# Kernel optimization log

Hardware: AMD Instinct MI355X
Metric: run time of the kernel (lower is better)

The kernel has to match this reference:

```python
import jax, jax.numpy as jnp
import numpy as np

N = 32768        # nodes (512 boards x 64 squares)
E_PER = 16384    # edges per edge type
T = 8            # edge types
IN = 16          # in_channels
H = 4            # attention heads
DIMS = (32, 128, 512)  # hidden_dim1, hidden_dim2, out_dim
NEG = 0.2        # LeakyReLU slope (PyG GATConv default)


def _glorot(key, shape):
    fan = shape[0] + shape[-1]
    return jax.random.uniform(key, shape, jnp.float32, -1.0, 1.0) * np.sqrt(6.0 / fan)


def setup_inputs() -> dict:
    key = jax.random.key(0)
    ki = iter(jax.random.split(key, 40))
    inp = {}
    inp["x"] = jax.random.normal(next(ki), (N, IN), jnp.float32)
    inp["edge_index_types"] = jax.random.randint(next(ki), (T, 2, E_PER), 0, N)
    in_dims = (IN,) + DIMS[:2]
    for l, (din, dout) in enumerate(zip(in_dims, DIMS), start=1):
        inp[f"W{l}"] = _glorot(next(ki), (din, H * dout))
        inp[f"We{l}"] = _glorot(next(ki), (T, H * dout))
        inp[f"asrc{l}"] = _glorot(next(ki), (H, dout))
        inp[f"adst{l}"] = _glorot(next(ki), (H, dout))
        inp[f"aedge{l}"] = _glorot(next(ki), (H, dout))
        inp[f"b{l}"] = jnp.zeros((dout,), jnp.float32)
    return inp


def _gat(h, src, dst, ea, W, We, a_src, a_dst, a_edge, b, dout):
    """One GATConv(heads=H, concat=False, edge_dim=T), inference (no dropout)."""
    hp = (h @ W).reshape(-1, H, dout)                 # [N,H,C]
    ep = (ea @ We).reshape(-1, H, dout)               # [E,H,C]
    alpha = ((hp * a_src).sum(-1)[src]
             + (hp * a_dst).sum(-1)[dst]
             + (ep * a_edge).sum(-1))                 # [E,H]
    alpha = jax.nn.leaky_relu(alpha, NEG)
    # scatter-softmax over incoming edges of each dst node
    m = jax.ops.segment_max(alpha, dst, num_segments=N)
    ex = jnp.exp(alpha - m[dst])
    denom = jax.ops.segment_sum(ex, dst, num_segments=N)
    w = ex / denom[dst]                               # [E,H]
    msg = hp[src] * w[:, :, None]                     # [E,H,C]
    out = jax.ops.segment_sum(msg, dst, num_segments=N)  # [N,H,C]
    return out.mean(axis=1) + b                       # concat=False -> head mean


def reference(x, edge_index_types, W1, We1, asrc1, adst1, aedge1, b1,
              W2, We2, asrc2, adst2, aedge2, b2,
              W3, We3, asrc3, adst3, aedge3, b3):
    # chess_graph_to_single: merge 8 edge lists, one-hot edge type attr
    ei = jnp.transpose(edge_index_types, (1, 0, 2)).reshape(2, T * E_PER)
    ea = jnp.repeat(jnp.eye(T, dtype=x.dtype), E_PER, axis=0)  # [T*E_PER, T]
    # PyG GATConv add_self_loops=True, fill_value='mean' for edge_attr
    loops = jnp.arange(N)
    src = jnp.concatenate([ei[0], loops])
    dst = jnp.concatenate([ei[1], loops])
    ea = jnp.concatenate([ea, jnp.broadcast_to(ea.mean(0), (N, T))], axis=0)

    h = jax.nn.relu(_gat(x, src, dst, ea, W1, We1, asrc1, adst1, aedge1, b1, DIMS[0]))
    h = jax.nn.relu(_gat(h, src, dst, ea, W2, We2, asrc2, adst2, aedge2, b2, DIMS[1]))
    return _gat(h, src, dst, ea, W3, We3, asrc3, adst3, aedge3, b3, DIMS[2])
```

## Files before the change

kernel.cpp:

```cpp
#include <hip/hip_runtime.h>
#include <hip/hip_bf16.h>
#include <math.h>

#define N_NODES 32768
#define E_PER   16384
#define T_TYPES 8
#define E_TYPED (T_TYPES * E_PER)
#define E_TOT   (E_TYPED + N_NODES)
#define NEG_SLOPE 0.2f
#define CSR_CAP 64

typedef _Float16 f16x8 __attribute__((ext_vector_type(8)));
typedef float f32x4 __attribute__((ext_vector_type(4)));

__device__ __forceinline__ float tof(float v) { return v; }
__device__ __forceinline__ float tof(_Float16 v) { return (float)v; }
__device__ __forceinline__ float lrelu(float a) { return a > 0.0f ? a : NEG_SLOPE * a; }

__device__ __forceinline__ void osm_upd(float& m, float& z, float a) {
  if (a > m) { z = z * __expf(m - a) + 1.0f; m = a; }
  else       { z += __expf(a - m); }
}
__device__ __forceinline__ void osm_comb(float& m, float& z, int off) {
  float om = __shfl_xor(m, off, 64);
  float oz = __shfl_xor(z, off, 64);
  float nm = fmaxf(m, om);
  z = z * __expf(m - nm) + oz * __expf(om - nm);
  m = nm;
}

__device__ __forceinline__ void gload16(const void* g, void* l) {
  __builtin_amdgcn_global_load_lds(
      (const __attribute__((address_space(1))) void*)g,
      (__attribute__((address_space(3))) void*)l,
      16, 0, 0);
}

__device__ void prep_blk(int b, const float* __restrict__ W, const float* __restrict__ We,
                         const float* __restrict__ asrc, const float* __restrict__ adst,
                         const float* __restrict__ aedge, float* __restrict__ prep,
                         int din, int dout) {
  int task = b * 4 + (threadIdx.x >> 6);
  int lane = threadIdx.x & 63;
  int hd = 4 * din;
  float s = 0.0f;
  if (task < 2 * hd) {
    int k = (task < hd) ? task : task - hd;
    int h = k / din, i = k % din;
    const float* a = (task < hd) ? asrc : adst;
    for (int c = lane; c < dout; c += 64)
      s += W[(size_t)i * 4 * dout + h * dout + c] * a[h * dout + c];
#pragma unroll
    for (int off = 32; off >= 1; off >>= 1) s += __shfl_xor(s, off, 64);
    if (lane == 0) prep[((task < hd) ? 0 : 512) + h * 128 + i] = s;
  } else if (task < 2 * hd + 32) {
    int k = task - 2 * hd; int t = k >> 2, h = k & 3;
    for (int c = lane; c < dout; c += 64)
      s += We[(size_t)t * 4 * dout + h * dout + c] * aedge[h * dout + c];
#pragma unroll
    for (int off = 32; off >= 1; off >>= 1) s += __shfl_xor(s, off, 64);
    if (lane == 0) prep[1024 + t * 4 + h] = s;
  } else if (task < 2 * hd + 36) {
    int h = task - 2 * hd - 32;
    for (int t = 0; t < 8; ++t)
      for (int c = lane; c < dout; c += 64)
        s += We[(size_t)t * 4 * dout + h * dout + c] * aedge[h * dout + c];
#pragma unroll
    for (int off = 32; off >= 1; off >>= 1) s += __shfl_xor(s, off, 64);
    if (lane == 0) prep[1024 + 32 + h] = s * 0.125f;
  }
}

__device__ void wt_blk(int jt, int kt, const float* __restrict__ W,
                       _Float16* __restrict__ Bt, int din, int dout) {
  __shared__ float Tt[64][65];
  int jb = jt * 64, kb = kt * 64;
  int KK = 4 * din;
  int tx = threadIdx.x & 63, ty4 = threadIdx.x >> 6;
  for (int r0 = 0; r0 < 64; r0 += 4) {
    int r = r0 + ty4;
    int k = kb + r, h = k / din, i = k % din;
    Tt[r][tx] = W[(size_t)i * 4 * dout + h * dout + jb + tx];
  }
  __syncthreads();
  for (int r0 = 0; r0 < 64; r0 += 4) {
    int r = r0 + ty4;
    Bt[(size_t)(jb + r) * KK + kb + tx] = (_Float16)Tt[tx][r];
  }
}

#define NB_P1 41
#define NB_P2 73
#define NB_P3 265
#define NB_W2 4
#define NB_W3 64
#define NB_Z  32
#define NB_WEIGHTS (NB_P1 + NB_P2 + NB_P3 + NB_W2 + NB_W3 + NB_Z)

__global__ __launch_bounds__(256) void k_weights(
    const float* __restrict__ W1, const float* __restrict__ We1,
    const float* __restrict__ as1, const float* __restrict__ ad1, const float* __restrict__ ae1,
    const float* __restrict__ W2, const float* __restrict__ We2,
    const float* __restrict__ as2, const float* __restrict__ ad2, const float* __restrict__ ae2,
    const float* __restrict__ W3, const float* __restrict__ We3,
    const float* __restrict__ as3, const float* __restrict__ ad3, const float* __restrict__ ae3,
    float* __restrict__ prep1, float* __restrict__ prep2, float* __restrict__ prep3,
    _Float16* __restrict__ w2t, _Float16* __restrict__ w3t, int* __restrict__ cnt) {
  int b = blockIdx.x;
  if (b < NB_P1) { prep_blk(b, W1, We1, as1, ad1, ae1, prep1, 16, 32); return; }
  b -= NB_P1;
  if (b < NB_P2) { prep_blk(b, W2, We2, as2, ad2, ae2, prep2, 32, 128); return; }
  b -= NB_P2;
  if (b < NB_P3) { prep_blk(b, W3, We3, as3, ad3, ae3, prep3, 128, 512); return; }
  b -= NB_P3;
  if (b < NB_W2) { wt_blk(b & 1, b >> 1, W2, w2t, 32, 128); return; }
  b -= NB_W2;
  if (b < NB_W3) { wt_blk(b & 7, b >> 3, W3, w3t, 128, 512); return; }
  b -= NB_W3;
  int4 z; z.x = z.y = z.z = z.w = 0;
  reinterpret_cast<int4*>(cnt)[b * 256 + threadIdx.x] = z;
}

__global__ __launch_bounds__(256) void k_fill_s1(const int* __restrict__ ei, int* __restrict__ cnt,
                                                 int* __restrict__ csr,
                                                 const float* __restrict__ x,
                                                 const float* __restrict__ prep1,
                                                 float* __restrict__ s_src,
                                                 float* __restrict__ s_dst) {
  int b = blockIdx.x;
  if (b < E_TOT / 256) {
    int e = b * 256 + threadIdx.x;
    int src, dst, t;
    if (e < E_TYPED) { t = e >> 14; int j = e & (E_PER - 1); src = ei[2 * t * E_PER + j]; dst = ei[(2 * t + 1) * E_PER + j]; }
    else { src = dst = e - E_TYPED; t = 8; }
    dst &= (N_NODES - 1);
    int pos = atomicAdd(cnt + dst, 1);
    if (pos < CSR_CAP)
      csr[dst * CSR_CAP + pos] = (src & (N_NODES - 1)) | (t << 16);
    return;
  }
  __shared__ float vv[128];
  int tid = threadIdx.x;
  for (int j = tid; j < 128; j += 256) {
    int s = j / 16, i = j % 16;
    vv[j] = prep1[(s & 3) * 128 + i + ((s >= 4) ? 512 : 0)];
  }
  __syncthreads();
  int lane = tid & 63, wv = tid >> 6;
  int n = (b - E_TOT / 256) * 4 + wv;
  const float* row = x + (size_t)n * 16;
  float p0 = 0, p1 = 0, p2 = 0, p3 = 0, p4 = 0, p5 = 0, p6 = 0, p7 = 0;
  for (int c = lane; c < 16; c += 64) {
    float v = row[c];
    p0 += v * vv[0 * 16 + c]; p1 += v * vv[1 * 16 + c];
    p2 += v * vv[2 * 16 + c]; p3 += v * vv[3 * 16 + c];
    p4 += v * vv[4 * 16 + c]; p5 += v * vv[5 * 16 + c];
    p6 += v * vv[6 * 16 + c]; p7 += v * vv[7 * 16 + c];
  }
#pragma unroll
  for (int off = 32; off >= 1; off >>= 1) {
    p0 += __shfl_xor(p0, off, 64); p1 += __shfl_xor(p1, off, 64);
    p2 += __shfl_xor(p2, off, 64); p3 += __shfl_xor(p3, off, 64);
    p4 += __shfl_xor(p4, off, 64); p5 += __shfl_xor(p5, off, 64);
    p6 += __shfl_xor(p6, off, 64); p7 += __shfl_xor(p7, off, 64);
  }
  if (lane == 0) {
    float* a = s_src + (size_t)n * 4; a[0] = p0; a[1] = p1; a[2] = p2; a[3] = p3;
    float* bq = s_dst + (size_t)n * 4; bq[0] = p4; bq[1] = p5; bq[2] = p6; bq[3] = p7;
  }
}

template <typename TI, int DIN, typename TO>
__global__ __launch_bounds__(256) void k_attn_agg(const TI* __restrict__ hin,
                                                  const int* __restrict__ csr,
                                                  const int* __restrict__ cnt,
                                                  const float* __restrict__ prep,
                                                  const float* __restrict__ s_src,
                                                  const float* __restrict__ s_dst,
                                                  TO* __restrict__ agg) {
  constexpr int ACC = (4 * DIN) / 64;
  __shared__ float se[68];
  int tid = threadIdx.x, lane = tid & 63, wv = tid >> 6;
  for (int j = tid; j < 68; j += 256) se[j] = (j < 36) ? prep[1024 + j] : 0.0f;
  __syncthreads();
  int n = blockIdx.x * 4 + wv;
  int o0 = n * CSR_CAP;
  int kd = cnt[n];
  kd = max(0, min(kd, CSR_CAP));
  const float* sdp = s_dst + (size_t)n * 4;
  float sd0 = sdp[0], sd1 = sdp[1], sd2 = sdp[2], sd3 = sdp[3];

  float m0 = -1e30f, m1 = -1e30f, m2 = -1e30f, m3 = -1e30f;
  float z0 = 0, z1 = 0, z2 = 0, z3 = 0;
  for (int i = lane; i < kd; i += 64) {
    int ent = csr[o0 + i];
    int sx = ent & (N_NODES - 1);
    int tt = (ent >> 16) & 15;
    const float4 sv = *reinterpret_cast<const float4*>(s_src + (size_t)sx * 4);
    float a0 = lrelu(sv.x + sd0 + se[tt * 4 + 0]);
    float a1 = lrelu(sv.y + sd1 + se[tt * 4 + 1]);
    float a2 = lrelu(sv.z + sd2 + se[tt * 4 + 2]);
    float a3 = lrelu(sv.w + sd3 + se[tt * 4 + 3]);
    osm_upd(m0, z0, a0); osm_upd(m1, z1, a1); osm_upd(m2, z2, a2); osm_upd(m3, z3, a3);
  }
#pragma unroll
  for (int off = 32; off >= 1; off >>= 1) {
    osm_comb(m0, z0, off); osm_comb(m1, z1, off);
    osm_comb(m2, z2, off); osm_comb(m3, z3, off);
  }
  float r0 = (z0 > 0.0f) ? 1.0f / z0 : 0.0f;
  float r1 = (z1 > 0.0f) ? 1.0f / z1 : 0.0f;
  float r2 = (z2 > 0.0f) ? 1.0f / z2 : 0.0f;
  float r3 = (z3 > 0.0f) ? 1.0f / z3 : 0.0f;

  float acc[ACC];
#pragma unroll
  for (int q = 0; q < ACC; ++q) acc[q] = 0.0f;

  for (int b0 = 0; b0 < kd; b0 += 64) {
    int i = b0 + lane;
    int sx = 0; float w0 = 0, w1 = 0, w2 = 0, w3 = 0;
    if (i < kd) {
      int ent = csr[o0 + i];
      sx = ent & (N_NODES - 1);
      int tt = (ent >> 16) & 15;
      const float4 sv = *reinterpret_cast<const float4*>(s_src + (size_t)sx * 4);
      w0 = __expf(lrelu(sv.x + sd0 + se[tt * 4 + 0]) - m0) * r0;
      w1 = __expf(lrelu(sv.y + sd1 + se[tt * 4 + 1]) - m1) * r1;
      w2 = __expf(lrelu(sv.z + sd2 + se[tt * 4 + 2]) - m2) * r2;
      w3 = __expf(lrelu(sv.w + sd3 + se[tt * 4 + 3]) - m3) * r3;
    }
    int cnt_ = min(64, kd - b0);
    for (int e = 0; e < cnt_; ++e) {
      int se_ = __shfl(sx, e, 64);
      float u0 = __shfl(w0, e, 64), u1 = __shfl(w1, e, 64);
      float u2 = __shfl(w2, e, 64), u3 = __shfl(w3, e, 64);
      if constexpr (DIN == 128) {
        unsigned int ru = *reinterpret_cast<const unsigned int*>(
            reinterpret_cast<const char*>(hin) + (size_t)se_ * 256 + 4 * lane);
        union { unsigned int u; _Float16 h[2]; } cv; cv.u = ru;
        float v0 = (float)cv.h[0], v1 = (float)cv.h[1];
        acc[0] += u0 * v0; acc[1] += u0 * v1;
        acc[2] += u1 * v0; acc[3] += u1 * v1;
        acc[4] += u2 * v0; acc[5] += u2 * v1;
        acc[6] += u3 * v0; acc[7] += u3 * v1;
      } else if constexpr (DIN == 32) {
        const TI* row = hin + (size_t)se_ * DIN;
        float v = tof(row[lane & 31]);
        bool hi = lane >= 32;
        float wa = hi ? u1 : u0;
        float wb = hi ? u3 : u2;
        acc[0] += wa * v; acc[1] += wb * v;
      } else {
        const TI* row = hin + (size_t)se_ * DIN;
        float v = tof(row[lane & 15]);
        int hh = lane >> 4;
        float wa = (hh == 0) ? u0 : (hh == 1) ? u1 : (hh == 2) ? u2 : u3;
        acc[0] += wa * v;
      }
    }
  }

  TO* ar = agg + (size_t)n * (4 * DIN);
  if constexpr (DIN == 128) {
#pragma unroll
    for (int h = 0; h < 4; ++h) {
      ar[h * 128 + 2 * lane]     = (TO)acc[2 * h];
      ar[h * 128 + 2 * lane + 1] = (TO)acc[2 * h + 1];
    }
  } else if constexpr (DIN == 32) {
    ar[lane]      = (TO)acc[0];
    ar[64 + lane] = (TO)acc[1];
  } else {
    ar[lane] = (TO)acc[0];
  }
}

__global__ __launch_bounds__(128) void k_gemm1_s2(const float* __restrict__ A,
                                                  const float* __restrict__ W,
                                                  const float* __restrict__ bias,
                                                  const float* __restrict__ prep2,
                                                  float* __restrict__ out,
                                                  float* __restrict__ s_src,
                                                  float* __restrict__ s_dst) {
  constexpr int BM = 64, BN = 32, BK = 16, TM = 4, TN = 4, NT = 128;
  constexpr int K = 64, DIN = 16, DOUT = 32;
  constexpr int LDA = BM + 4;
  constexpr int LDB = BN + 4;
  __shared__ __align__(16) float As[BK * LDA];
  __shared__ __align__(16) float Bs[BK * LDB];
  __shared__ float ot[64][33];
  const int tid = threadIdx.x;
  const int tx = tid % (BN / TN);
  const int ty = tid / (BN / TN);
  const int mb = blockIdx.y * BM;
  float acc[TM][TN] = {};
  constexpr int ITA = (BM * BK) / (NT * 4);
  constexpr int ITB = (BK * BN) / (NT * 4);
  for (int kb = 0; kb < K; kb += BK) {
#pragma unroll
    for (int it = 0; it < ITA; ++it) {
      int f = it * NT * 4 + tid * 4;
      int r = f / BK, c = f % BK;
      float4 u = *reinterpret_cast<const float4*>(A + (size_t)(mb + r) * K + kb + c);
      As[(c + 0) * LDA + r] = u.x;
      As[(c + 1) * LDA + r] = u.y;
      As[(c + 2) * LDA + r] = u.z;
      As[(c + 3) * LDA + r] = u.w;
    }
#pragma unroll
    for (int it = 0; it < ITB; ++it) {
      int f = it * NT * 4 + tid * 4;
      int kk = f / BN, jj = f % BN;
      int k = kb + kk; int h = k / DIN; int i = k % DIN;
      float4 u = *reinterpret_cast<const float4*>(W + (size_t)i * 4 * DOUT + h * DOUT + jj);
      Bs[kk * LDB + jj + 0] = u.x;
      Bs[kk * LDB + jj + 1] = u.y;
      Bs[kk * LDB + jj + 2] = u.z;
      Bs[kk * LDB + jj + 3] = u.w;
    }
    __syncthreads();
#pragma unroll
    for (int kk = 0; kk < BK; ++kk) {
      float a_[TM], b_[TN];
      float4 va = *reinterpret_cast<const float4*>(&As[kk * LDA + ty * TM]);
      a_[0] = va.x; a_[1] = va.y; a_[2] = va.z; a_[3] = va.w;
      float4 vb = *reinterpret_cast<const float4*>(&Bs[kk * LDB + tx * TN]);
      b_[0] = vb.x; b_[1] = vb.y; b_[2] = vb.z; b_[3] = vb.w;
#pragma unroll
      for (int ii = 0; ii < TM; ++ii)
#pragma unroll
        for (int jj = 0; jj < TN; ++jj)
          acc[ii][jj] = fmaf(a_[ii], b_[jj], acc[ii][jj]);
    }
    __syncthreads();
  }
#pragma unroll
  for (int ii = 0; ii < TM; ++ii) {
    int ml = ty * TM + ii;
#pragma unroll
    for (int jj = 0; jj < TN; ++jj) {
      int j = tx * TN + jj;
      float v = acc[ii][jj] * 0.25f + bias[j];
      v = fmaxf(v, 0.0f);
      if (!isfinite(v)) v = 0.0f;
      out[(size_t)(mb + ml) * DOUT + j] = v;
      ot[ml][j] = v;
    }
  }
  __syncthreads();
#pragma unroll
  for (int q = 0; q < 4; ++q) {
    int t = q * 128 + tid;
    int s = t & 7, row = t >> 3;
    const float* vp = prep2 + (s & 3) * 128 + ((s >= 4) ? 512 : 0);
    float p = 0.0f;
#pragma unroll
    for (int c = 0; c < 32; ++c) p += ot[row][c] * vp[c];
    int n = mb + row;
    if (s < 4) s_src[(size_t)n * 4 + s] = p;
    else       s_dst[(size_t)n * 4 + (s - 4)] = p;
  }
}

__global__ __launch_bounds__(256) void k_gemm2_s3(const _Float16* __restrict__ A,
                                                  const _Float16* __restrict__ Bt,
                                                  const float* __restrict__ bias,
                                                  const float* __restrict__ prep3,
                                                  _Float16* __restrict__ out,
                                                  float* __restrict__ s_src,
                                                  float* __restrict__ s_dst) {
  constexpr int K = 128, DOUT = 128, BM = 128, BK = 64;
  __shared__ _Float16 smem[128 * 136];
  _Float16* As = smem;
  _Float16* Bs = smem + 8192;
  const int tid = threadIdx.x;
  const int lane = tid & 63, wv = tid >> 6;
  const int quad = lane >> 4, l16 = lane & 15;
  const int wm = (wv >> 1) * 64, wn = (wv & 1) * 64;
  const int mb = blockIdx.y * BM;
  const int srow = lane >> 3;
  const int scolB = (lane & 7) * 16;

  f32x4 acc[4][4] = {};
  float bv[4];
#pragma unroll
  for (int fj = 0; fj < 4; ++fj) bv[fj] = bias[wn + fj * 16 + l16];

  for (int kb = 0; kb < K; kb += BK) {
    __syncthreads();
#pragma unroll
    for (int i = 0; i < 4; ++i) {
      int q = wv * 4 + i;
      int r = q * 8 + srow;
      gload16(reinterpret_cast<const char*>(A) + (size_t)(mb + r) * 256 + kb * 2 + scolB,
              &As[q * 512]);
      gload16(reinterpret_cast<const char*>(Bt) + (size_t)r * 256 + kb * 2 + scolB,
              &Bs[q * 512]);
    }
    __syncthreads();
#pragma unroll
    for (int h = 0; h < 2; ++h) {
      f16x8 af[4], bf[4];
#pragma unroll
      for (int f = 0; f < 4; ++f) {
        af[f] = *reinterpret_cast<const f16x8*>(&As[(wm + f * 16 + l16) * 64 + h * 32 + quad * 8]);
        bf[f] = *reinterpret_cast<const f16x8*>(&Bs[(wn + f * 16 + l16) * 64 + h * 32 + quad * 8]);
      }
#pragma unroll
      for (int fi = 0; fi < 4; ++fi)
#pragma unroll
        for (int fj = 0; fj < 4; ++fj)
          acc[fi][fj] = __builtin_amdgcn_mfma_f32_16x16x32_f16(af[fi], bf[fj], acc[fi][fj], 0, 0, 0);
    }
  }
  __syncthreads();
  _Float16* ot = smem;
#pragma unroll
  for (int fi = 0; fi < 4; ++fi)
#pragma unroll
    for (int reg = 0; reg < 4; ++reg) {
      int ml = wm + fi * 16 + quad * 4 + reg;
#pragma unroll
      for (int fj = 0; fj < 4; ++fj) {
        int j = wn + fj * 16 + l16;
        float v = acc[fi][fj][reg] * 0.25f + bv[fj];
        v = fmaxf(v, 0.0f);
        if (!isfinite(v)) v = 0.0f;
        _Float16 hv = (_Float16)v;
        out[(size_t)(mb + ml) * DOUT + j] = hv;
        ot[ml * 136 + j] = hv;
      }
    }
  __syncthreads();
#pragma unroll
  for (int q = 0; q < 4; ++q) {
    int t = q * 256 + tid;
    int s = t & 7, row = t >> 3;
    const float* vp = prep3 + (s & 3) * 128 + ((s >= 4) ? 512 : 0);
    float p = 0.0f;
#pragma unroll
    for (int c0 = 0; c0 < 128; c0 += 8) {
      f16x8 hv = *reinterpret_cast<const f16x8*>(&ot[row * 136 + c0]);
      float4 a0 = *reinterpret_cast<const float4*>(vp + c0);
      float4 a1 = *reinterpret_cast<const float4*>(vp + c0 + 4);
      p += (float)hv[0] * a0.x + (float)hv[1] * a0.y + (float)hv[2] * a0.z + (float)hv[3] * a0.w
         + (float)hv[4] * a1.x + (float)hv[5] * a1.y + (float)hv[6] * a1.z + (float)hv[7] * a1.w;
    }
    int n = mb + row;
    if (s < 4) s_src[(size_t)n * 4 + s] = p;
    else       s_dst[(size_t)n * 4 + (s - 4)] = p;
  }
}

template <int K, int DOUT, bool RELU, typename TO>
__global__ __launch_bounds__(256) void k_gemm_mfma64(const _Float16* __restrict__ A,
                                                     const _Float16* __restrict__ Bt,
                                                     const float* __restrict__ bias,
                                                     TO* __restrict__ out) {
  constexpr int BM = 128, BK = 64;
  __shared__ _Float16 As[128 * 64];
  __shared__ _Float16 Bs[128 * 64];
  const int tid = threadIdx.x;
  const int lane = tid & 63, wv = tid >> 6;
  const int quad = lane >> 4, l16 = lane & 15;
  const int wm = (wv >> 1) * 64, wn = (wv & 1) * 64;
  const int mb = blockIdx.y * BM, jb = blockIdx.x * BM;
  const int srow = lane >> 3;
  const int scolB = (lane & 7) * 16;
  constexpr int ROWB = K * 2;

  f32x4 acc[4][4] = {};
  float bv[4];
#pragma unroll
  for (int fj = 0; fj < 4; ++fj) bv[fj] = bias[jb + wn + fj * 16 + l16];

  for (int kb = 0; kb < K; kb += BK) {
    __syncthreads();
#pragma unroll
    for (int i = 0; i < 4; ++i) {
      int q = wv * 4 + i;
      int r = q * 8 + srow;
      gload16(reinterpret_cast<const char*>(A) + (size_t)(mb + r) * ROWB + kb * 2 + scolB,
              &As[q * 512]);
      gload16(reinterpret_cast<const char*>(Bt) + (size_t)(jb + r) * ROWB + kb * 2 + scolB,
              &Bs[q * 512]);
    }
    __syncthreads();
#pragma unroll
    for (int h = 0; h < 2; ++h) {
      f16x8 af[4], bf[4];
#pragma unroll
      for (int f = 0; f < 4; ++f) {
        af[f] = *reinterpret_cast<const f16x8*>(&As[(wm + f * 16 + l16) * 64 + h * 32 + quad * 8]);
        bf[f] = *reinterpret_cast<const f16x8*>(&Bs[(wn + f * 16 + l16) * 64 + h * 32 + quad * 8]);
      }
#pragma unroll
      for (int fi = 0; fi < 4; ++fi)
#pragma unroll
        for (int fj = 0; fj < 4; ++fj)
          acc[fi][fj] = __builtin_amdgcn_mfma_f32_16x16x32_f16(af[fi], bf[fj], acc[fi][fj], 0, 0, 0);
    }
  }
#pragma unroll
  for (int fi = 0; fi < 4; ++fi)
#pragma unroll
    for (int reg = 0; reg < 4; ++reg) {
      int m = mb + wm + fi * 16 + quad * 4 + reg;
#pragma unroll
      for (int fj = 0; fj < 4; ++fj) {
        int j = jb + wn + fj * 16 + l16;
        float v = acc[fi][fj][reg] * 0.25f + bv[fj];
        if (RELU) v = fmaxf(v, 0.0f);
        if (!isfinite(v)) v = 0.0f;
        out[(size_t)m * DOUT + j] = (TO)v;
      }
    }
}

extern "C" void kernel_launch(void* const* d_in, const int* in_sizes, int n_in,
                              void* d_out, int out_size, void* d_ws, size_t ws_size,
                              hipStream_t stream) {
  (void)in_sizes; (void)n_in; (void)out_size; (void)ws_size;
  const float* x   = (const float*)d_in[0];
  const int*   ei  = (const int*)d_in[1];
  const float* W1  = (const float*)d_in[2];
  const float* We1 = (const float*)d_in[3];
  const float* as1 = (const float*)d_in[4];
  const float* ad1 = (const float*)d_in[5];
  const float* ae1 = (const float*)d_in[6];
  const float* b1  = (const float*)d_in[7];
  const float* W2  = (const float*)d_in[8];
  const float* We2 = (const float*)d_in[9];
  const float* as2 = (const float*)d_in[10];
  const float* ad2 = (const float*)d_in[11];
  const float* ae2 = (const float*)d_in[12];
  const float* b2  = (const float*)d_in[13];
  const float* W3  = (const float*)d_in[14];
  const float* We3 = (const float*)d_in[15];
  const float* as3 = (const float*)d_in[16];
  const float* ad3 = (const float*)d_in[17];
  const float* ae3 = (const float*)d_in[18];
  const float* b3  = (const float*)d_in[19];

  char* p = (char*)d_ws;
  int* cnt       = (int*)(p + 0);
  int* csr       = (int*)(p + 131072);
  float* ssrc    = (float*)(p + 8519680);
  float* sdst    = (float*)(p + 9043968);
  float* prep1   = (float*)(p + 9568256);
  float* prep2   = (float*)(p + 9572864);
  float* prep3   = (float*)(p + 9577472);
  float* h1      = (float*)(p + 9582080);
  _Float16* h2   = (_Float16*)(p + 13776384);
  float* agg1    = (float*)(p + 22164992);
  _Float16* agg2 = (_Float16*)(p + 30553600);
  _Float16* agg3 = (_Float16*)(p + 38942208);
  _Float16* w2t  = (_Float16*)(p + 72496640);
  _Float16* w3t  = (_Float16*)(p + 72529408);

  k_weights<<<NB_WEIGHTS, 256, 0, stream>>>(W1, We1, as1, ad1, ae1,
                                            W2, We2, as2, ad2, ae2,
                                            W3, We3, as3, ad3, ae3,
                                            prep1, prep2, prep3, w2t, w3t, cnt);
  k_fill_s1<<<E_TOT / 256 + N_NODES / 4, 256, 0, stream>>>(ei, cnt, csr, x, prep1, ssrc, sdst);

  k_attn_agg<float, 16, float><<<N_NODES / 4, 256, 0, stream>>>(x, csr, cnt, prep1, ssrc, sdst, agg1);
  k_gemm1_s2<<<dim3(1, N_NODES / 64), 128, 0, stream>>>(agg1, W1, b1, prep2, h1, ssrc, sdst);

  k_attn_agg<float, 32, _Float16><<<N_NODES / 4, 256, 0, stream>>>(h1, csr, cnt, prep2, ssrc, sdst, agg2);
  k_gemm2_s3<<<dim3(1, N_NODES / 128), 256, 0, stream>>>(agg2, w2t, b2, prep3, h2, ssrc, sdst);

  k_attn_agg<_Float16, 128, _Float16><<<N_NODES / 4, 256, 0, stream>>>(h2, csr, cnt, prep3, ssrc, sdst, agg3);
  k_gemm_mfma64<512, 512, false, float>
      <<<dim3(4, N_NODES / 128), 256, 0, stream>>>(agg3, w3t, b3, (float*)d_out);
}
```

Measured before the change: 319.0 us.

## Fuse all GAT stages into one persistent kernel with grid barriers

Replaces the eight separate launches with one persistent kernel of 512 blocks that steps through weight prep, CSR build, and the three attention-aggregate plus GEMM layers, separated by software grid barriers. Layers 1 and 2 now run aggregation and the dense transform in the same block, so the agg1/agg2 intermediates never go to global memory. The attention scores are double-buffered so one layer's scores can be written while the previous layer's are still being read. This removes per-launch overhead and some global round trips, but it relies on all 512 blocks being resident at once and on spin-wait barriers, and the final GEMM switches to smaller 64-row tiles.

```diff
diff --git a/kernel.cpp b/kernel.cpp
--- a/kernel.cpp
+++ b/kernel.cpp
@@ -9,18 +9,13 @@
 #define E_TOT   (E_TYPED + N_NODES)
 #define NEG_SLOPE 0.2f
 #define CSR_CAP 64
+#define GRID 512
 
 typedef _Float16 f16x8 __attribute__((ext_vector_type(8)));
 typedef float f32x4 __attribute__((ext_vector_type(4)));
 
-__device__ __forceinline__ float tof(float v) { return v; }
-__device__ __forceinline__ float tof(_Float16 v) { return (float)v; }
 __device__ __forceinline__ float lrelu(float a) { return a > 0.0f ? a : NEG_SLOPE * a; }
 
-__device__ __forceinline__ void osm_upd(float& m, float& z, float a) {
-  if (a > m) { z = z * __expf(m - a) + 1.0f; m = a; }
-  else       { z += __expf(a - m); }
-}
 __device__ __forceinline__ void osm_comb(float& m, float& z, int off) {
   float om = __shfl_xor(m, off, 64);
   float oz = __shfl_xor(z, off, 64);
@@ -34,6 +29,21 @@
       (const __attribute__((address_space(1))) void*)g,
       (__attribute__((address_space(3))) void*)l,
       16, 0, 0);
+}
+
+__device__ __forceinline__ void gridbar(int* bar, int target) {
+  __threadfence();
+  __syncthreads();
+  if (threadIdx.x == 0) {
+    atomicAdd(bar, 1);
+    int it = 0;
+    while (__hip_atomic_load(bar, __ATOMIC_RELAXED, __HIP_MEMORY_SCOPE_AGENT) < target) {
+      __builtin_amdgcn_s_sleep(2);
+      if (++it > (1 << 24)) break;
+    }
+  }
+  __syncthreads();
+  __threadfence();
 }
 
 __device__ void prep_blk(int b, const float* __restrict__ W, const float* __restrict__ We,
@@ -72,21 +82,21 @@
 }
 
 __device__ void wt_blk(int jt, int kt, const float* __restrict__ W,
-                       _Float16* __restrict__ Bt, int din, int dout) {
-  __shared__ float Tt[64][65];
+                       _Float16* __restrict__ Bt, int din, int dout, float* T) {
   int jb = jt * 64, kb = kt * 64;
   int KK = 4 * din;
   int tx = threadIdx.x & 63, ty4 = threadIdx.x >> 6;
   for (int r0 = 0; r0 < 64; r0 += 4) {
     int r = r0 + ty4;
     int k = kb + r, h = k / din, i = k % din;
-    Tt[r][tx] = W[(size_t)i * 4 * dout + h * dout + jb + tx];
+    T[r * 65 + tx] = W[(size_t)i * 4 * dout + h * dout + jb + tx];
   }
   __syncthreads();
   for (int r0 = 0; r0 < 64; r0 += 4) {
     int r = r0 + ty4;
-    Bt[(size_t)(jb + r) * KK + kb + tx] = (_Float16)Tt[tx][r];
-  }
+    Bt[(size_t)(jb + r) * KK + kb + tx] = (_Float16)T[tx * 65 + r];
+  }
+  __syncthreads();
 }
 
 #define NB_P1 41
@@ -96,426 +106,436 @@
 #define NB_W3 64
 #define NB_Z  32
 #define NB_WEIGHTS (NB_P1 + NB_P2 + NB_P3 + NB_W2 + NB_W3 + NB_Z)
-
-__global__ __launch_bounds__(256) void k_weights(
+#define NB_FILL 640
+#define NB_S1 8192
+
+__global__ __launch_bounds__(256, 2) void k_mega(
+    const float* __restrict__ x, const int* __restrict__ ei,
     const float* __restrict__ W1, const float* __restrict__ We1,
     const float* __restrict__ as1, const float* __restrict__ ad1, const float* __restrict__ ae1,
+    const float* __restrict__ b1,
     const float* __restrict__ W2, const float* __restrict__ We2,
     const float* __restrict__ as2, const float* __restrict__ ad2, const float* __restrict__ ae2,
+    const float* __restrict__ b2,
     const float* __restrict__ W3, const float* __restrict__ We3,
     const float* __restrict__ as3, const float* __restrict__ ad3, const float* __restrict__ ae3,
+    const float* __restrict__ b3,
+    int* __restrict__ cnt, int* __restrict__ csr,
+    float* __restrict__ ssrcA, float* __restrict__ sdstA,
+    float* __restrict__ ssrcB, float* __restrict__ sdstB,
     float* __restrict__ prep1, float* __restrict__ prep2, float* __restrict__ prep3,
-    _Float16* __restrict__ w2t, _Float16* __restrict__ w3t, int* __restrict__ cnt) {
-  int b = blockIdx.x;
-  if (b < NB_P1) { prep_blk(b, W1, We1, as1, ad1, ae1, prep1, 16, 32); return; }
-  b -= NB_P1;
-  if (b < NB_P2) { prep_blk(b, W2, We2, as2, ad2, ae2, prep2, 32, 128); return; }
-  b -= NB_P2;
-  if (b < NB_P3) { prep_blk(b, W3, We3, as3, ad3, ae3, prep3, 128, 512); return; }
-  b -= NB_P3;
-  if (b < NB_W2) { wt_blk(b & 1, b >> 1, W2, w2t, 32, 128); return; }
-  b -= NB_W2;
-  if (b < NB_W3) { wt_blk(b & 7, b >> 3, W3, w3t, 128, 512); return; }
-  b -= NB_W3;
-  int4 z; z.x = z.y = z.z = z.w = 0;
-  reinterpret_cast<int4*>(cnt)[b * 256 + threadIdx.x] = z;
-}
-
-__global__ __launch_bounds__(256) void k_fill_s1(const int* __restrict__ ei, int* __restrict__ cnt,
-                                                 int* __restrict__ csr,
-                                                 const float* __restrict__ x,
-                                                 const float* __restrict__ prep1,
-                                                 float* __restrict__ s_src,
-                                                 float* __restrict__ s_dst) {
-  int b = blockIdx.x;
-  if (b < E_TOT / 256) {
-    int e = b * 256 + threadIdx.x;
-    int src, dst, t;
-    if (e < E_TYPED) { t = e >> 14; int j = e & (E_PER - 1); src = ei[2 * t * E_PER + j]; dst = ei[(2 * t + 1) * E_PER + j]; }
-    else { src = dst = e - E_TYPED; t = 8; }
-    dst &= (N_NODES - 1);
-    int pos = atomicAdd(cnt + dst, 1);
-    if (pos < CSR_CAP)
-      csr[dst * CSR_CAP + pos] = (src & (N_NODES - 1)) | (t << 16);
-    return;
-  }
-  __shared__ float vv[128];
-  int tid = threadIdx.x;
-  for (int j = tid; j < 128; j += 256) {
-    int s = j / 16, i = j % 16;
-    vv[j] = prep1[(s & 3) * 128 + i + ((s >= 4) ? 512 : 0)];
-  }
-  __syncthreads();
-  int lane = tid & 63, wv = tid >> 6;
-  int n = (b - E_TOT / 256) * 4 + wv;
-  const float* row = x + (size_t)n * 16;
-  float p0 = 0, p1 = 0, p2 = 0, p3 = 0, p4 = 0, p5 = 0, p6 = 0, p7 = 0;
-  for (int c = lane; c < 16; c += 64) {
-    float v = row[c];
-    p0 += v * vv[0 * 16 + c]; p1 += v * vv[1 * 16 + c];
-    p2 += v * vv[2 * 16 + c]; p3 += v * vv[3 * 16 + c];
-    p4 += v * vv[4 * 16 + c]; p5 += v * vv[5 * 16 + c];
-    p6 += v * vv[6 * 16 + c]; p7 += v * vv[7 * 16 + c];
-  }
-#pragma unroll
-  for (int off = 32; off >= 1; off >>= 1) {
-    p0 += __shfl_xor(p0, off, 64); p1 += __shfl_xor(p1, off, 64);
-    p2 += __shfl_xor(p2, off, 64); p3 += __shfl_xor(p3, off, 64);
-    p4 += __shfl_xor(p4, off, 64); p5 += __shfl_xor(p5, off, 64);
-    p6 += __shfl_xor(p6, off, 64); p7 += __shfl_xor(p7, off, 64);
-  }
-  if (lane == 0) {
-    float* a = s_src + (size_t)n * 4; a[0] = p0; a[1] = p1; a[2] = p2; a[3] = p3;
-    float* bq = s_dst + (size_t)n * 4; bq[0] = p4; bq[1] = p5; bq[2] = p6; bq[3] = p7;
-  }
-}
-
-template <typename TI, int DIN, typename TO>
-__global__ __launch_bounds__(256) void k_attn_agg(const TI* __restrict__ hin,
-                                                  const int* __restrict__ csr,
-                                                  const int* __restrict__ cnt,
-                                                  const float* __restrict__ prep,
-                                                  const float* __restrict__ s_src,
-                                                  const float* __restrict__ s_dst,
-                                                  TO* __restrict__ agg) {
-  constexpr int ACC = (4 * DIN) / 64;
-  __shared__ float se[68];
-  int tid = threadIdx.x, lane = tid & 63, wv = tid >> 6;
-  for (int j = tid; j < 68; j += 256) se[j] = (j < 36) ? prep[1024 + j] : 0.0f;
-  __syncthreads();
-  int n = blockIdx.x * 4 + wv;
-  int o0 = n * CSR_CAP;
-  int kd = cnt[n];
-  kd = max(0, min(kd, CSR_CAP));
-  const float* sdp = s_dst + (size_t)n * 4;
-  float sd0 = sdp[0], sd1 = sdp[1], sd2 = sdp[2], sd3 = sdp[3];
-
-  float m0 = -1e30f, m1 = -1e30f, m2 = -1e30f, m3 = -1e30f;
-  float z0 = 0, z1 = 0, z2 = 0, z3 = 0;
-  for (int i = lane; i < kd; i += 64) {
-    int ent = csr[o0 + i];
-    int sx = ent & (N_NODES - 1);
-    int tt = (ent >> 16) & 15;
-    const float4 sv = *reinterpret_cast<const float4*>(s_src + (size_t)sx * 4);
-    float a0 = lrelu(sv.x + sd0 + se[tt * 4 + 0]);
-    float a1 = lrelu(sv.y + sd1 + se[tt * 4 + 1]);
-    float a2 = lrelu(sv.z + sd2 + se[tt * 4 + 2]);
-    float a3 = lrelu(sv.w + sd3 + se[tt * 4 + 3]);
-    osm_upd(m0, z0, a0); osm_upd(m1, z1, a1); osm_upd(m2, z2, a2); osm_upd(m3, z3, a3);
-  }
-#pragma unroll
-  for (int off = 32; off >= 1; off >>= 1) {
-    osm_comb(m0, z0, off); osm_comb(m1, z1, off);
-    osm_comb(m2, z2, off); osm_comb(m3, z3, off);
-  }
-  float r0 = (z0 > 0.0f) ? 1.0f / z0 : 0.0f;
-  float r1 = (z1 > 0.0f) ? 1.0f / z1 : 0.0f;
-  float r2 = (z2 > 0.0f) ? 1.0f / z2 : 0.0f;
-  float r3 = (z3 > 0.0f) ? 1.0f / z3 : 0.0f;
-
-  float acc[ACC];
-#pragma unroll
-  for (int q = 0; q < ACC; ++q) acc[q] = 0.0f;
-
-  for (int b0 = 0; b0 < kd; b0 += 64) {
-    int i = b0 + lane;
-    int sx = 0; float w0 = 0, w1 = 0, w2 = 0, w3 = 0;
-    if (i < kd) {
-      int ent = csr[o0 + i];
-      sx = ent & (N_NODES - 1);
-      int tt = (ent >> 16) & 15;
-      const float4 sv = *reinterpret_cast<const float4*>(s_src + (size_t)sx * 4);
-      w0 = __expf(lrelu(sv.x + sd0 + se[tt * 4 + 0]) - m0) * r0;
-      w1 = __expf(lrelu(sv.y + sd1 + se[tt * 4 + 1]) - m1) * r1;
-      w2 = __expf(lrelu(sv.z + sd2 + se[tt * 4 + 2]) - m2) * r2;
-      w3 = __expf(lrelu(sv.w + sd3 + se[tt * 4 + 3]) - m3) * r3;
-    }
-    int cnt_ = min(64, kd - b0);
-    for (int e = 0; e < cnt_; ++e) {
-      int se_ = __shfl(sx, e, 64);
-      float u0 = __shfl(w0, e, 64), u1 = __shfl(w1, e, 64);
-      float u2 = __shfl(w2, e, 64), u3 = __shfl(w3, e, 64);
-      if constexpr (DIN == 128) {
+    float* __restrict__ h1, _Float16* __restrict__ h2, _Float16* __restrict__ agg3,
+    _Float16* __restrict__ w2t, _Float16* __restrict__ w3t,
+    float* __restrict__ dout, int* bar) {
+  __shared__ __align__(16) char LB[34304];
+  const int tid = threadIdx.x;
+  const int lane = tid & 63, wv = tid >> 6;
+  const int quad = lane >> 4, l16 = lane & 15;
+  const int srow = lane >> 3, scolB = (lane & 7) * 16;
+  const int wm = (wv >> 1) * 32, wn = (wv & 1) * 64;
+
+  for (int vb = blockIdx.x; vb < NB_WEIGHTS; vb += GRID) {
+    int b = vb;
+    if (b < NB_P1) { prep_blk(b, W1, We1, as1, ad1, ae1, prep1, 16, 32); continue; }
+    b -= NB_P1;
+    if (b < NB_P2) { prep_blk(b, W2, We2, as2, ad2, ae2, prep2, 32, 128); continue; }
+    b -= NB_P2;
+    if (b < NB_P3) { prep_blk(b, W3, We3, as3, ad3, ae3, prep3, 128, 512); continue; }
+    b -= NB_P3;
+    if (b < NB_W2) { wt_blk(b & 1, b >> 1, W2, w2t, 32, 128, (float*)LB); continue; }
+    b -= NB_W2;
+    if (b < NB_W3) { wt_blk(b & 7, b >> 3, W3, w3t, 128, 512, (float*)LB); continue; }
+    b -= NB_W3;
+    int4 z; z.x = z.y = z.z = z.w = 0;
+    reinterpret_cast<int4*>(cnt)[b * 256 + tid] = z;
+  }
+  gridbar(bar, 1 * GRID);
+
+  {
+    float* vv = (float*)(LB + 33792);
+    for (int j = tid; j < 128; j += 256) {
+      int s = j >> 4, i = j & 15;
+      vv[j] = prep1[(s & 3) * 128 + i + ((s >= 4) ? 512 : 0)];
+    }
+    __syncthreads();
+    for (int vb = blockIdx.x; vb < NB_FILL + NB_S1; vb += GRID) {
+      if (vb < NB_FILL) {
+        int e = vb * 256 + tid;
+        int src, dst, t;
+        if (e < E_TYPED) { t = e >> 14; int j = e & (E_PER - 1); src = ei[2 * t * E_PER + j]; dst = ei[(2 * t + 1) * E_PER + j]; }
+        else { src = dst = e - E_TYPED; t = 8; }
+        dst &= (N_NODES - 1);
+        int pos = atomicAdd(cnt + dst, 1);
+        if (pos < CSR_CAP)
+          csr[dst * CSR_CAP + pos] = (src & (N_NODES - 1)) | (t << 16);
+      } else {
+        int n = (vb - NB_FILL) * 4 + wv;
+        const float* row = x + (size_t)n * 16;
+        float p0 = 0, p1 = 0, p2 = 0, p3 = 0, p4 = 0, p5 = 0, p6 = 0, p7 = 0;
+        for (int c = lane; c < 16; c += 64) {
+          float v = row[c];
+          p0 += v * vv[0 * 16 + c]; p1 += v * vv[1 * 16 + c];
+          p2 += v * vv[2 * 16 + c]; p3 += v * vv[3 * 16 + c];
+          p4 += v * vv[4 * 16 + c]; p5 += v * vv[5 * 16 + c];
+          p6 += v * vv[6 * 16 + c]; p7 += v * vv[7 * 16 + c];
+        }
+#pragma unroll
+        for (int off = 32; off >= 1; off >>= 1) {
+          p0 += __shfl_xor(p0, off, 64); p1 += __shfl_xor(p1, off, 64);
+          p2 += __shfl_xor(p2, off, 64); p3 += __shfl_xor(p3, off, 64);
+          p4 += __shfl_xor(p4, off, 64); p5 += __shfl_xor(p5, off, 64);
+          p6 += __shfl_xor(p6, off, 64); p7 += __shfl_xor(p7, off, 64);
+        }
+        if (lane == 0) {
+          float* a = ssrcA + (size_t)n * 4; a[0] = p0; a[1] = p1; a[2] = p2; a[3] = p3;
+          float* bq = sdstA + (size_t)n * 4; bq[0] = p4; bq[1] = p5; bq[2] = p6; bq[3] = p7;
+        }
+      }
+    }
+  }
+  gridbar(bar, 2 * GRID);
+
+  {
+    float* Asf = (float*)LB;
+    float* Bsf = (float*)(LB + 17408);
+    float* se_ = (float*)(LB + 33792);
+    const int nb = blockIdx.x * 64;
+    for (int j = tid; j < 40; j += 256) se_[j] = (j < 36) ? prep1[1024 + j] : 0.0f;
+    for (int idx = tid; idx < 2048; idx += 256) {
+      int k = idx >> 5, j = idx & 31, h = k >> 4, i = k & 15;
+      Bsf[k * 36 + j] = W1[i * 128 + h * 32 + j];
+    }
+    __syncthreads();
+    for (int g = 0; g < 16; ++g) {
+      int nl = wv * 16 + g, n = nb + nl;
+      int kd = min(cnt[n], CSR_CAP);
+      int o0 = n * CSR_CAP;
+      const float* sdp = sdstA + (size_t)n * 4;
+      float sd0 = sdp[0], sd1 = sdp[1], sd2 = sdp[2], sd3 = sdp[3];
+      float a0 = -1e30f, a1 = -1e30f, a2 = -1e30f, a3 = -1e30f;
+      float m0 = -1e30f, m1 = -1e30f, m2 = -1e30f, m3 = -1e30f;
+      float z0 = 0, z1 = 0, z2 = 0, z3 = 0;
+      int sx = 0;
+      if (lane < kd) {
+        int ent = csr[o0 + lane];
+        sx = ent & (N_NODES - 1);
+        int tt = (ent >> 16) & 15;
+        const float4 sv = *reinterpret_cast<const float4*>(ssrcA + (size_t)sx * 4);
+        a0 = lrelu(sv.x + sd0 + se_[tt * 4 + 0]);
+        a1 = lrelu(sv.y + sd1 + se_[tt * 4 + 1]);
+        a2 = lrelu(sv.z + sd2 + se_[tt * 4 + 2]);
+        a3 = lrelu(sv.w + sd3 + se_[tt * 4 + 3]);
+        m0 = a0; m1 = a1; m2 = a2; m3 = a3;
+        z0 = 1; z1 = 1; z2 = 1; z3 = 1;
+      }
+#pragma unroll
+      for (int off = 32; off >= 1; off >>= 1) {
+        osm_comb(m0, z0, off); osm_comb(m1, z1, off);
+        osm_comb(m2, z2, off); osm_comb(m3, z3, off);
+      }
+      float r0 = (z0 > 0.0f) ? 1.0f / z0 : 0.0f;
+      float r1 = (z1 > 0.0f) ? 1.0f / z1 : 0.0f;
+      float r2 = (z2 > 0.0f) ? 1.0f / z2 : 0.0f;
+      float r3 = (z3 > 0.0f) ? 1.0f / z3 : 0.0f;
+      float w0 = 0, w1 = 0, w2 = 0, w3 = 0;
+      if (lane < kd) {
+        w0 = __expf(a0 - m0) * r0; w1 = __expf(a1 - m1) * r1;
+        w2 = __expf(a2 - m2) * r2; w3 = __expf(a3 - m3) * r3;
+      }
+      float acc = 0.0f;
+      for (int e = 0; e < kd; ++e) {
+        int se2 = __shfl(sx, e, 64);
+        float u0 = __shfl(w0, e, 64), u1 = __shfl(w1, e, 64);
+        float u2 = __shfl(w2, e, 64), u3 = __shfl(w3, e, 64);
+        float v = x[(size_t)se2 * 16 + (lane & 15)];
+        int hh = lane >> 4;
+        float wa = (hh == 0) ? u0 : (hh == 1) ? u1 : (hh == 2) ? u2 : u3;
+        acc += wa * v;
+      }
+      Asf[nl * 68 + lane] = acc;
+    }
+    __syncthreads();
+    int m = tid >> 2, j0 = (tid & 3) * 8;
+    float a8[8] = {};
+    for (int kk = 0; kk < 64; ++kk) {
+      float a = Asf[m * 68 + kk];
+#pragma unroll
+      for (int q = 0; q < 8; ++q) a8[q] = fmaf(a, Bsf[kk * 36 + j0 + q], a8[q]);
+    }
+    __syncthreads();
+    float* ot = Asf;
+#pragma unroll
+    for (int q = 0; q < 8; ++q) {
+      float v = a8[q] * 0.25f + b1[j0 + q];
+      v = fmaxf(v, 0.0f);
+      if (!isfinite(v)) v = 0.0f;
+      h1[(size_t)(nb + m) * 32 + j0 + q] = v;
+      ot[m * 33 + j0 + q] = v;
+    }
+    __syncthreads();
+#pragma unroll
+    for (int q = 0; q < 2; ++q) {
+      int t = q * 256 + tid;
+      int s = t & 7, row = t >> 3;
+      const float* vp = prep2 + (s & 3) * 128 + ((s >= 4) ? 512 : 0);
+      float p = 0.0f;
+#pragma unroll
+      for (int c = 0; c < 32; ++c) p += ot[row * 33 + c] * vp[c];
+      int n = nb + row;
+      if (s < 4) ssrcB[(size_t)n * 4 + s] = p;
+      else       sdstB[(size_t)n * 4 + (s - 4)] = p;
+    }
+  }
+  gridbar(bar, 3 * GRID);
+
+  {
+    _Float16* As16 = (_Float16*)LB;
+    _Float16* Bs16 = (_Float16*)(LB + 17408);
+    float* se_ = (float*)(LB + 33792);
+    const int nb = blockIdx.x * 64;
+    for (int j = tid; j < 40; j += 256) se_[j] = (j < 36) ? prep2[1024 + j] : 0.0f;
+    __syncthreads();
+    for (int g = 0; g < 16; ++g) {
+      int nl = wv * 16 + g, n = nb + nl;
+      int kd = min(cnt[n], CSR_CAP);
+      int o0 = n * CSR_CAP;
+      const float* sdp = sdstB + (size_t)n * 4;
+      float sd0 = sdp[0], sd1 = sdp[1], sd2 = sdp[2], sd3 = sdp[3];
+      float a0 = -1e30f, a1 = -1e30f, a2 = -1e30f, a3 = -1e30f;
+      float m0 = -1e30f, m1 = -1e30f, m2 = -1e30f, m3 = -1e30f;
+      float z0 = 0, z1 = 0, z2 = 0, z3 = 0;
+      int sx = 0;
+      if (lane < kd) {
+        int ent = csr[o0 + lane];
+        sx = ent & (N_NODES - 1);
+        int tt = (ent >> 16) & 15;
+        const float4 sv = *reinterpret_cast<const float4*>(ssrcB + (size_t)sx * 4);
+        a0 = lrelu(sv.x + sd0 + se_[tt * 4 + 0]);
+        a1 = lrelu(sv.y + sd1 + se_[tt * 4 + 1]);
+        a2 = lrelu(sv.z + sd2 + se_[tt * 4 + 2]);
+        a3 = lrelu(sv.w + sd3 + se_[tt * 4 + 3]);
+        m0 = a0; m1 = a1; m2 = a2; m3 = a3;
+        z0 = 1; z1 = 1; z2 = 1; z3 = 1;
+      }
+#pragma unroll
+      for (int off = 32; off >= 1; off >>= 1) {
+        osm_comb(m0, z0, off); osm_comb(m1, z1, off);
+        osm_comb(m2, z2, off); osm_comb(m3, z3, off);
+      }
+      float r0 = (z0 > 0.0f) ? 1.0f / z0 : 0.0f;
+      float r1 = (z1 > 0.0f) ? 1.0f / z1 : 0.0f;
+      float r2 = (z2 > 0.0f) ? 1.0f / z2 : 0.0f;
+      float r3 = (z3 > 0.0f) ? 1.0f / z3 : 0.0f;
+      float w0 = 0, w1 = 0, w2 = 0, w3 = 0;
+      if (lane < kd) {
+        w0 = __expf(a0 - m0) * r0; w1 = __expf(a1 - m1) * r1;
+        w2 = __expf(a2 - m2) * r2; w3 = __expf(a3 - m3) * r3;
+      }
+      float ac0 = 0.0f, ac1 = 0.0f;
+      for (int e = 0; e < kd; ++e) {
+        int se2 = __shfl(sx, e, 64);
+        float u0 = __shfl(w0, e, 64), u1 = __shfl(w1, e, 64);
+        float u2 = __shfl(w2, e, 64), u3 = __shfl(w3, e, 64);
+        float v = h1[(size_t)se2 * 32 + (lane & 31)];
+        bool hi = lane >= 32;
+        float wa = hi ? u1 : u0;
+        float wb = hi ? u3 : u2;
+        ac0 += wa * v; ac1 += wb * v;
+      }
+      As16[nl * 136 + lane]      = (_Float16)ac0;
+      As16[nl * 136 + 64 + lane] = (_Float16)ac1;
+    }
+    __syncthreads();
+    float bv[4];
+#pragma unroll
+    for (int fj = 0; fj < 4; ++fj) bv[fj] = b2[wn + fj * 16 + l16];
+    f32x4 acc[2][4] = {};
+    for (int kb = 0; kb < 128; kb += 64) {
+      __syncthreads();
+#pragma unroll
+      for (int i = 0; i < 4; ++i) {
+        int q = wv * 4 + i, r = q * 8 + srow;
+        gload16(reinterpret_cast<const char*>(w2t) + (size_t)r * 256 + kb * 2 + scolB,
+                &Bs16[q * 512]);
+      }
+      __syncthreads();
+#pragma unroll
+      for (int h = 0; h < 2; ++h) {
+        f16x8 af[2], bf[4];
+#pragma unroll
+        for (int f = 0; f < 2; ++f)
+          af[f] = *reinterpret_cast<const f16x8*>(&As16[(wm + f * 16 + l16) * 136 + kb + h * 32 + quad * 8]);
+#pragma unroll
+        for (int f = 0; f < 4; ++f)
+          bf[f] = *reinterpret_cast<const f16x8*>(&Bs16[(wn + f * 16 + l16) * 64 + h * 32 + quad * 8]);
+#pragma unroll
+        for (int fi = 0; fi < 2; ++fi)
+#pragma unroll
+          for (int fj = 0; fj < 4; ++fj)
+            acc[fi][fj] = __builtin_amdgcn_mfma_f32_16x16x32_f16(af[fi], bf[fj], acc[fi][fj], 0, 0, 0);
+      }
+    }
+    __syncthreads();
+    _Float16* ot16 = As16;
+#pragma unroll
+    for (int fi = 0; fi < 2; ++fi)
+#pragma unroll
+      for (int reg = 0; reg < 4; ++reg) {
+        int ml = wm + fi * 16 + quad * 4 + reg;
+#pragma unroll
+        for (int fj = 0; fj < 4; ++fj) {
+          int j = wn + fj * 16 + l16;
+          float v = acc[fi][fj][reg] * 0.25f + bv[fj];
+          v = fmaxf(v, 0.0f);
+          if (!isfinite(v)) v = 0.0f;
+          _Float16 hv = (_Float16)v;
+          h2[(size_t)(nb + ml) * 128 + j] = hv;
+          ot16[ml * 136 + j] = hv;
+        }
+      }
+    __syncthreads();
+#pragma unroll
+    for (int q = 0; q < 2; ++q) {
+      int t = q * 256 + tid;
+      int s = t & 7, row = t >> 3;
+      const float* vp = prep3 + (s & 3) * 128 + ((s >= 4) ? 512 : 0);
+      float p = 0.0f;
+#pragma unroll
+      for (int c0 = 0; c0 < 128; c0 += 8) {
+        f16x8 hv = *reinterpret_cast<const f16x8*>(&ot16[row * 136 + c0]);
+        float4 q0 = *reinterpret_cast<const float4*>(vp + c0);
+        float4 q1 = *reinterpret_cast<const float4*>(vp + c0 + 4);
+        p += (float)hv[0] * q0.x + (float)hv[1] * q0.y + (float)hv[2] * q0.z + (float)hv[3] * q0.w
+           + (float)hv[4] * q1.x + (float)hv[5] * q1.y + (float)hv[6] * q1.z + (float)hv[7] * q1.w;
+      }
+      int n = nb + row;
+      if (s < 4) ssrcA[(size_t)n * 4 + s] = p;
+      else       sdstA[(size_t)n * 4 + (s - 4)] = p;
+    }
+  }
+  gridbar(bar, 4 * GRID);
+
+  {
+    float* se_ = (float*)(LB + 33792);
+    for (int j = tid; j < 40; j += 256) se_[j] = (j < 36) ? prep3[1024 + j] : 0.0f;
+    __syncthreads();
+    for (int vb = blockIdx.x; vb < 8192; vb += GRID) {
+      int n = vb * 4 + wv;
+      int kd = min(cnt[n], CSR_CAP);
+      int o0 = n * CSR_CAP;
+      const float* sdp = sdstA + (size_t)n * 4;
+      float sd0 = sdp[0], sd1 = sdp[1], sd2 = sdp[2], sd3 = sdp[3];
+      float a0 = -1e30f, a1 = -1e30f, a2 = -1e30f, a3 = -1e30f;
+      float m0 = -1e30f, m1 = -1e30f, m2 = -1e30f, m3 = -1e30f;
+      float z0 = 0, z1 = 0, z2 = 0, z3 = 0;
+      int sx = 0;
+      if (lane < kd) {
+        int ent = csr[o0 + lane];
+        sx = ent & (N_NODES - 1);
+        int tt = (ent >> 16) & 15;
+        const float4 sv = *reinterpret_cast<const float4*>(ssrcA + (size_t)sx * 4);
+        a0 = lrelu(sv.x + sd0 + se_[tt * 4 + 0]);
+        a1 = lrelu(sv.y + sd1 + se_[tt * 4 + 1]);
+        a2 = lrelu(sv.z + sd2 + se_[tt * 4 + 2]);
+        a3 = lrelu(sv.w + sd3 + se_[tt * 4 + 3]);
+        m0 = a0; m1 = a1; m2 = a2; m3 = a3;
+        z0 = 1; z1 = 1; z2 = 1; z3 = 1;
+      }
+#pragma unroll
+      for (int off = 32; off >= 1; off >>= 1) {
+        osm_comb(m0, z0, off); osm_comb(m1, z1, off);
+        osm_comb(m2, z2, off); osm_comb(m3, z3, off);
+      }
+      float r0 = (z0 > 0.0f) ? 1.0f / z0 : 0.0f;
+      float r1 = (z1 > 0.0f) ? 1.0f / z1 : 0.0f;
+      float r2 = (z2 > 0.0f) ? 1.0f / z2 : 0.0f;
+      float r3 = (z3 > 0.0f) ? 1.0f / z3 : 0.0f;
+      float w0 = 0, w1 = 0, w2 = 0, w3 = 0;
+      if (lane < kd) {
+        w0 = __expf(a0 - m0) * r0; w1 = __expf(a1 - m1) * r1;
+        w2 = __expf(a2 - m2) * r2; w3 = __expf(a3 - m3) * r3;
+      }
+      float acc[8] = {};
+      for (int e = 0; e < kd; ++e) {
+        int se2 = __shfl(sx, e, 64);
+        float u0 = __shfl(w0, e, 64), u1 = __shfl(w1, e, 64);
+        float u2 = __shfl(w2, e, 64), u3 = __shfl(w3, e, 64);
         unsigned int ru = *reinterpret_cast<const unsigned int*>(
-            reinterpret_cast<const char*>(hin) + (size_t)se_ * 256 + 4 * lane);
-        union { unsigned int u; _Float16 h[2]; } cv; cv.u = ru;
-        float v0 = (float)cv.h[0], v1 = (float)cv.h[1];
+            reinterpret_cast<const char*>(h2) + (size_t)se2 * 256 + 4 * lane);
+        union { unsigned int u; _Float16 hh[2]; } cv; cv.u = ru;
+        float v0 = (float)cv.hh[0], v1 = (float)cv.hh[1];
         acc[0] += u0 * v0; acc[1] += u0 * v1;
         acc[2] += u1 * v0; acc[3] += u1 * v1;
         acc[4] += u2 * v0; acc[5] += u2 * v1;
         acc[6] += u3 * v0; acc[7] += u3 * v1;
-      } else if constexpr (DIN == 32) {
-        const TI* row = hin + (size_t)se_ * DIN;
-        float v = tof(row[lane & 31]);
-        bool hi = lane >= 32;
-        float wa = hi ? u1 : u0;
-        float wb = hi ? u3 : u2;
-        acc[0] += wa * v; acc[1] += wb * v;
-      } else {
-        const TI* row = hin + (size_t)se_ * DIN;
-        float v = tof(row[lane & 15]);
-        int hh = lane >> 4;
-        float wa = (hh == 0) ? u0 : (hh == 1) ? u1 : (hh == 2) ? u2 : u3;
-        acc[0] += wa * v;
-      }
-    }
-  }
-
-  TO* ar = agg + (size_t)n * (4 * DIN);
-  if constexpr (DIN == 128) {
-#pragma unroll
-    for (int h = 0; h < 4; ++h) {
-      ar[h * 128 + 2 * lane]     = (TO)acc[2 * h];
-      ar[h * 128 + 2 * lane + 1] = (TO)acc[2 * h + 1];
-    }
-  } else if constexpr (DIN == 32) {
-    ar[lane]      = (TO)acc[0];
-    ar[64 + lane] = (TO)acc[1];
-  } else {
-    ar[lane] = (TO)acc[0];
-  }
-}
-
-__global__ __launch_bounds__(128) void k_gemm1_s2(const float* __restrict__ A,
-                                                  const float* __restrict__ W,
-                                                  const float* __restrict__ bias,
-                                                  const float* __restrict__ prep2,
-                                                  float* __restrict__ out,
-                                                  float* __restrict__ s_src,
-                                                  float* __restrict__ s_dst) {
-  constexpr int BM = 64, BN = 32, BK = 16, TM = 4, TN = 4, NT = 128;
-  constexpr int K = 64, DIN = 16, DOUT = 32;
-  constexpr int LDA = BM + 4;
-  constexpr int LDB = BN + 4;
-  __shared__ __align__(16) float As[BK * LDA];
-  __shared__ __align__(16) float Bs[BK * LDB];
-  __shared__ float ot[64][33];
-  const int tid = threadIdx.x;
-  const int tx = tid % (BN / TN);
-  const int ty = tid / (BN / TN);
-  const int mb = blockIdx.y * BM;
-  float acc[TM][TN] = {};
-  constexpr int ITA = (BM * BK) / (NT * 4);
-  constexpr int ITB = (BK * BN) / (NT * 4);
-  for (int kb = 0; kb < K; kb += BK) {
-#pragma unroll
-    for (int it = 0; it < ITA; ++it) {
-      int f = it * NT * 4 + tid * 4;
-      int r = f / BK, c = f % BK;
-      float4 u = *reinterpret_cast<const float4*>(A + (size_t)(mb + r) * K + kb + c);
-      As[(c + 0) * LDA + r] = u.x;
-      As[(c + 1) * LDA + r] = u.y;
-      As[(c + 2) * LDA + r] = u.z;
-      As[(c + 3) * LDA + r] = u.w;
-    }
-#pragma unroll
-    for (int it = 0; it < ITB; ++it) {
-      int f = it * NT * 4 + tid * 4;
-      int kk = f / BN, jj = f % BN;
-      int k = kb + kk; int h = k / DIN; int i = k % DIN;
-      float4 u = *reinterpret_cast<const float4*>(W + (size_t)i * 4 * DOUT + h * DOUT + jj);
-      Bs[kk * LDB + jj + 0] = u.x;
-      Bs[kk * LDB + jj + 1] = u.y;
-      Bs[kk * LDB + jj + 2] = u.z;
-      Bs[kk * LDB + jj + 3] = u.w;
-    }
-    __syncthreads();
-#pragma unroll
-    for (int kk = 0; kk < BK; ++kk) {
-      float a_[TM], b_[TN];
-      float4 va = *reinterpret_cast<const float4*>(&As[kk * LDA + ty * TM]);
-      a_[0] = va.x; a_[1] = va.y; a_[2] = va.z; a_[3] = va.w;
-      float4 vb = *reinterpret_cast<const float4*>(&Bs[kk * LDB + tx * TN]);
-      b_[0] = vb.x; b_[1] = vb.y; b_[2] = vb.z; b_[3] = vb.w;
-#pragma unroll
-      for (int ii = 0; ii < TM; ++ii)
-#pragma unroll
-        for (int jj = 0; jj < TN; ++jj)
-          acc[ii][jj] = fmaf(a_[ii], b_[jj], acc[ii][jj]);
-    }
-    __syncthreads();
-  }
-#pragma unroll
-  for (int ii = 0; ii < TM; ++ii) {
-    int ml = ty * TM + ii;
-#pragma unroll
-    for (int jj = 0; jj < TN; ++jj) {
-      int j = tx * TN + jj;
-      float v = acc[ii][jj] * 0.25f + bias[j];
-      v = fmaxf(v, 0.0f);
-      if (!isfinite(v)) v = 0.0f;
-      out[(size_t)(mb + ml) * DOUT + j] = v;
-      ot[ml][j] = v;
-    }
-  }
-  __syncthreads();
-#pragma unroll
-  for (int q = 0; q < 4; ++q) {
-    int t = q * 128 + tid;
-    int s = t & 7, row = t >> 3;
-    const float* vp = prep2 + (s & 3) * 128 + ((s >= 4) ? 512 : 0);
-    float p = 0.0f;
-#pragma unroll
-    for (int c = 0; c < 32; ++c) p += ot[row][c] * vp[c];
-    int n = mb + row;
-    if (s < 4) s_src[(size_t)n * 4 + s] = p;
-    else       s_dst[(size_t)n * 4 + (s - 4)] = p;
-  }
-}
-
-__global__ __launch_bounds__(256) void k_gemm2_s3(const _Float16* __restrict__ A,
-                                                  const _Float16* __restrict__ Bt,
-                                                  const float* __restrict__ bias,
-                                                  const float* __restrict__ prep3,
-                                                  _Float16* __restrict__ out,
-                                                  float* __restrict__ s_src,
-                                                  float* __restrict__ s_dst) {
-  constexpr int K = 128, DOUT = 128, BM = 128, BK = 64;
-  __shared__ _Float16 smem[128 * 136];
-  _Float16* As = smem;
-  _Float16* Bs = smem + 8192;
-  const int tid = threadIdx.x;
-  const int lane = tid & 63, wv = tid >> 6;
-  const int quad = lane >> 4, l16 = lane & 15;
-  const int wm = (wv >> 1) * 64, wn = (wv & 1) * 64;
-  const int mb = blockIdx.y * BM;
-  const int srow = lane >> 3;
-  const int scolB = (lane & 7) * 16;
-
-  f32x4 acc[4][4] = {};
-  float bv[4];
-#pragma unroll
-  for (int fj = 0; fj < 4; ++fj) bv[fj] = bias[wn + fj * 16 + l16];
-
-  for (int kb = 0; kb < K; kb += BK) {
-    __syncthreads();
-#pragma unroll
-    for (int i = 0; i < 4; ++i) {
-      int q = wv * 4 + i;
-      int r = q * 8 + srow;
-      gload16(reinterpret_cast<const char*>(A) + (size_t)(mb + r) * 256 + kb * 2 + scolB,
-              &As[q * 512]);
-      gload16(reinterpret_cast<const char*>(Bt) + (size_t)r * 256 + kb * 2 + scolB,
-              &Bs[q * 512]);
-    }
-    __syncthreads();
-#pragma unroll
-    for (int h = 0; h < 2; ++h) {
-      f16x8 af[4], bf[4];
-#pragma unroll
-      for (int f = 0; f < 4; ++f) {
-        af[f] = *reinterpret_cast<const f16x8*>(&As[(wm + f * 16 + l16) * 64 + h * 32 + quad * 8]);
-        bf[f] = *reinterpret_cast<const f16x8*>(&Bs[(wn + f * 16 + l16) * 64 + h * 32 + quad * 8]);
-      }
-#pragma unroll
-      for (int fi = 0; fi < 4; ++fi)
-#pragma unroll
-        for (int fj = 0; fj < 4; ++fj)
-          acc[fi][fj] = __builtin_amdgcn_mfma_f32_16x16x32_f16(af[fi], bf[fj], acc[fi][fj], 0, 0, 0);
-    }
-  }
-  __syncthreads();
-  _Float16* ot = smem;
-#pragma unroll
-  for (int fi = 0; fi < 4; ++fi)
-#pragma unroll
-    for (int reg = 0; reg < 4; ++reg) {
-      int ml = wm + fi * 16 + quad * 4 + reg;
-#pragma unroll
-      for (int fj = 0; fj < 4; ++fj) {
-        int j = wn + fj * 16 + l16;
-        float v = acc[fi][fj][reg] * 0.25f + bv[fj];
-        v = fmaxf(v, 0.0f);
-        if (!isfinite(v)) v = 0.0f;
-        _Float16 hv = (_Float16)v;
-        out[(size_t)(mb + ml) * DOUT + j] = hv;
-        ot[ml * 136 + j] = hv;
-      }
-    }
-  __syncthreads();
-#pragma unroll
-  for (int q = 0; q < 4; ++q) {
-    int t = q * 256 + tid;
-    int s = t & 7, row = t >> 3;
-    const float* vp = prep3 + (s & 3) * 128 + ((s >= 4) ? 512 : 0);
-    float p = 0.0f;
-#pragma unroll
-    for (int c0 = 0; c0 < 128; c0 += 8) {
-      f16x8 hv = *reinterpret_cast<const f16x8*>(&ot[row * 136 + c0]);
-      float4 a0 = *reinterpret_cast<const float4*>(vp + c0);
-      float4 a1 = *reinterpret_cast<const float4*>(vp + c0 + 4);
-      p += (float)hv[0] * a0.x + (float)hv[1] * a0.y + (float)hv[2] * a0.z + (float)hv[3] * a0.w
-         + (float)hv[4] * a1.x + (float)hv[5] * a1.y + (float)hv[6] * a1.z + (float)hv[7] * a1.w;
-    }
-    int n = mb + row;
-    if (s < 4) s_src[(size_t)n * 4 + s] = p;
-    else       s_dst[(size_t)n * 4 + (s - 4)] = p;
-  }
-}
-
-template <int K, int DOUT, bool RELU, typename TO>
-__global__ __launch_bounds__(256) void k_gemm_mfma64(const _Float16* __restrict__ A,
-                                                     const _Float16* __restrict__ Bt,
-                                                     const float* __restrict__ bias,
-                                                     TO* __restrict__ out) {
-  constexpr int BM = 128, BK = 64;
-  __shared__ _Float16 As[128 * 64];
-  __shared__ _Float16 Bs[128 * 64];
-  const int tid = threadIdx.x;
-  const int lane = tid & 63, wv = tid >> 6;
-  const int quad = lane >> 4, l16 = lane & 15;
-  const int wm = (wv >> 1) * 64, wn = (wv & 1) * 64;
-  const int mb = blockIdx.y * BM, jb = blockIdx.x * BM;
-  const int srow = lane >> 3;
-  const int scolB = (lane & 7) * 16;
-  constexpr int ROWB = K * 2;
-
-  f32x4 acc[4][4] = {};
-  float bv[4];
-#pragma unroll
-  for (int fj = 0; fj < 4; ++fj) bv[fj] = bias[jb + wn + fj * 16 + l16];
-
-  for (int kb = 0; kb < K; kb += BK) {
-    __syncthreads();
-#pragma unroll
-    for (int i = 0; i < 4; ++i) {
-      int q = wv * 4 + i;
-      int r = q * 8 + srow;
-      gload16(reinterpret_cast<const char*>(A) + (size_t)(mb + r) * ROWB + kb * 2 + scolB,
-              &As[q * 512]);
-      gload16(reinterpret_cast<const char*>(Bt) + (size_t)(jb + r) * ROWB + kb * 2 + scolB,
-              &Bs[q * 512]);
-    }
-    __syncthreads();
-#pragma unroll
-    for (int h = 0; h < 2; ++h) {
-      f16x8 af[4], bf[4];
-#pragma unroll
-      for (int f = 0; f < 4; ++f) {
-        af[f] = *reinterpret_cast<const f16x8*>(&As[(wm + f * 16 + l16) * 64 + h * 32 + quad * 8]);
-        bf[f] = *reinterpret_cast<const f16x8*>(&Bs[(wn + f * 16 + l16) * 64 + h * 32 + quad * 8]);
-      }
-#pragma unroll
-      for (int fi = 0; fi < 4; ++fi)
-#pragma unroll
-        for (int fj = 0; fj < 4; ++fj)
-          acc[fi][fj] = __builtin_amdgcn_mfma_f32_16x16x32_f16(af[fi], bf[fj], acc[fi][fj], 0, 0, 0);
-    }
-  }
-#pragma unroll
-  for (int fi = 0; fi < 4; ++fi)
-#pragma unroll
-    for (int reg = 0; reg < 4; ++reg) {
-      int m = mb + wm + fi * 16 + quad * 4 + reg;
-#pragma unroll
-      for (int fj = 0; fj < 4; ++fj) {
-        int j = jb + wn + fj * 16 + l16;
-        float v = acc[fi][fj][reg] * 0.25f + bv[fj];
-        if (RELU) v = fmaxf(v, 0.0f);
-        if (!isfinite(v)) v = 0.0f;
-        out[(size_t)m * DOUT + j] = (TO)v;
-      }
-    }
+      }
+      _Float16* ar = agg3 + (size_t)n * 512;
+#pragma unroll
+      for (int h = 0; h < 4; ++h) {
+        union { unsigned int u; _Float16 hh[2]; } ov;
+        ov.hh[0] = (_Float16)acc[2 * h]; ov.hh[1] = (_Float16)acc[2 * h + 1];
+        *reinterpret_cast<unsigned int*>(ar + h * 128 + 2 * lane) = ov.u;
+      }
+    }
+  }
+  gridbar(bar, 5 * GRID);
+
+  {
+    _Float16* As16 = (_Float16*)LB;
+    _Float16* Bs16 = (_Float16*)(LB + 8192);
+    for (int vb = blockIdx.x; vb < 2048; vb += GRID) {
+      const int ct = vb & 3, rt = vb >> 2;
+      const int mb = rt * 64, jb = ct * 128;
+      float bv[4];
+#pragma unroll
+      for (int fj = 0; fj < 4; ++fj) bv[fj] = b3[jb + wn + fj * 16 + l16];
+      f32x4 acc[2][4] = {};
+      for (int kb = 0; kb < 512; kb += 64) {
+        __syncthreads();
+#pragma unroll
+        for (int i = 0; i < 2; ++i) {
+          int q = wv * 2 + i, r = q * 8 + srow;
+          gload16(reinterpret_cast<const char*>(agg3) + (size_t)(mb + r) * 1024 + kb * 2 + scolB,
+                  &As16[q * 512]);
+        }
+#pragma unroll
+        for (int i = 0; i < 4; ++i) {
+          int q = wv * 4 + i, r = q * 8 + srow;
+          gload16(reinterpret_cast<const char*>(w3t) + (size_t)(jb + r) * 1024 + kb * 2 + scolB,
+                  &Bs16[q * 512]);
+        }
+        __syncthreads();
+#pragma unroll
+        for (int h = 0; h < 2; ++h) {
+          f16x8 af[2], bf[4];
+#pragma unroll
+          for (int f = 0; f < 2; ++f)
+            af[f] = *reinterpret_cast<const f16x8*>(&As16[(wm + f * 16 + l16) * 64 + h * 32 + quad * 8]);
+#pragma unroll
+          for (int f = 0; f < 4; ++f)
+            bf[f] = *reinterpret_cast<const f16x8*>(&Bs16[(wn + f * 16 + l16) * 64 + h * 32 + quad * 8]);
+#pragma unroll
+          for (int fi = 0; fi < 2; ++fi)
+#pragma unroll
+            for (int fj = 0; fj < 4; ++fj)
+              acc[fi][fj] = __builtin_amdgcn_mfma_f32_16x16x32_f16(af[fi], bf[fj], acc[fi][fj], 0, 0, 0);
+        }
+      }
+#pragma unroll
+      for (int fi = 0; fi < 2; ++fi)
+#pragma unroll
+        for (int reg = 0; reg < 4; ++reg) {
+          int m = mb + wm + fi * 16 + quad * 4 + reg;
+#pragma unroll
+          for (int fj = 0; fj < 4; ++fj) {
+            int j = jb + wn + fj * 16 + l16;
+            float v = acc[fi][fj][reg] * 0.25f + bv[fj];
+            if (!isfinite(v)) v = 0.0f;
+            dout[(size_t)m * 512 + j] = v;
+          }
+        }
+    }
+  }
 }
 
 extern "C" void kernel_launch(void* const* d_in, const int* in_sizes, int n_in,
@@ -546,32 +566,26 @@
   char* p = (char*)d_ws;
   int* cnt       = (int*)(p + 0);
   int* csr       = (int*)(p + 131072);
-  float* ssrc    = (float*)(p + 8519680);
-  float* sdst    = (float*)(p + 9043968);
-  float* prep1   = (float*)(p + 9568256);
-  float* prep2   = (float*)(p + 9572864);
-  float* prep3   = (float*)(p + 9577472);
-  float* h1      = (float*)(p + 9582080);
-  _Float16* h2   = (_Float16*)(p + 13776384);
-  float* agg1    = (float*)(p + 22164992);
-  _Float16* agg2 = (_Float16*)(p + 30553600);
-  _Float16* agg3 = (_Float16*)(p + 38942208);
-  _Float16* w2t  = (_Float16*)(p + 72496640);
-  _Float16* w3t  = (_Float16*)(p + 72529408);
-
-  k_weights<<<NB_WEIGHTS, 256, 0, stream>>>(W1, We1, as1, ad1, ae1,
-                                            W2, We2, as2, ad2, ae2,
-                                            W3, We3, as3, ad3, ae3,
-                                            prep1, prep2, prep3, w2t, w3t, cnt);
-  k_fill_s1<<<E_TOT / 256 + N_NODES / 4, 256, 0, stream>>>(ei, cnt, csr, x, prep1, ssrc, sdst);
-
-  k_attn_agg<float, 16, float><<<N_NODES / 4, 256, 0, stream>>>(x, csr, cnt, prep1, ssrc, sdst, agg1);
-  k_gemm1_s2<<<dim3(1, N_NODES / 64), 128, 0, stream>>>(agg1, W1, b1, prep2, h1, ssrc, sdst);
-
-  k_attn_agg<float, 32, _Float16><<<N_NODES / 4, 256, 0, stream>>>(h1, csr, cnt, prep2, ssrc, sdst, agg2);
-  k_gemm2_s3<<<dim3(1, N_NODES / 128), 256, 0, stream>>>(agg2, w2t, b2, prep3, h2, ssrc, sdst);
-
-  k_attn_agg<_Float16, 128, _Float16><<<N_NODES / 4, 256, 0, stream>>>(h2, csr, cnt, prep3, ssrc, sdst, agg3);
-  k_gemm_mfma64<512, 512, false, float>
-      <<<dim3(4, N_NODES / 128), 256, 0, stream>>>(agg3, w3t, b3, (float*)d_out);
-}
+  float* ssrcA   = (float*)(p + 8519680);
+  float* sdstA   = (float*)(p + 9043968);
+  float* ssrcB   = (float*)(p + 9568256);
+  float* sdstB   = (float*)(p + 10092544);
+  float* prep1   = (float*)(p + 10616832);
+  float* prep2   = (float*)(p + 10621440);
+  float* prep3   = (float*)(p + 10626048);
+  float* h1      = (float*)(p + 10630656);
+  _Float16* h2   = (_Float16*)(p + 14824960);
+  _Float16* agg3 = (_Float16*)(p + 23213568);
+  _Float16* w2t  = (_Float16*)(p + 56768000);
+  _Float16* w3t  = (_Float16*)(p + 56800768);
+  int* bar       = (int*)(p + 57325056);
+
+  hipMemsetAsync(bar, 0, 256, stream);
+  k_mega<<<GRID, 256, 0, stream>>>(x, ei,
+                                   W1, We1, as1, ad1, ae1, b1,
+                                   W2, We2, as2, ad2, ae2, b2,
+                                   W3, We3, as3, ad3, ae3, b3,
+                                   cnt, csr, ssrcA, sdstA, ssrcB, sdstB,
+                                   prep1, prep2, prep3, h1, h2, agg3, w2t, w3t,
+                                   (float*)d_out, bar);
+}
```

After: 897.6 us. 181% more time.
